# Kernel tuning notes

Measured on AMD Instinct MI355X. Metric: run time of the kernel, lower is better.

## Reference

```python
import jax, jax.numpy as jnp
import numpy as np

T = 2048          # num tokens (prefill)
H = 4096          # hidden_size
NH = 32           # num query heads
NKV = 8           # num kv heads (GQA)
HD = H // NH      # head_dim = 128
BASE = 1000000.0  # rope_theta
NEG = -1e30


def _rope(x, positions):
    # NeoX-style rotary embedding (vLLM default). x: [T, nh, HD]
    half = HD // 2
    inv_freq = 1.0 / (BASE ** (jnp.arange(half, dtype=jnp.float32) / half))
    freqs = positions.astype(jnp.float32)[:, None] * inv_freq  # [T, half]
    cos = jnp.concatenate([jnp.cos(freqs), jnp.cos(freqs)], -1)[:, None, :]
    sin = jnp.concatenate([jnp.sin(freqs), jnp.sin(freqs)], -1)[:, None, :]
    rot = jnp.concatenate([-x[..., half:], x[..., :half]], -1)
    return x * cos + rot * sin


def setup_inputs() -> dict:
    key = jax.random.key(0)
    k1, k2, k3 = jax.random.split(key, 3)
    hidden_states = jax.random.normal(k1, (T, H), jnp.float32)
    wqkv = jax.random.normal(k2, (H, (NH + 2 * NKV) * HD), jnp.float32) * 0.02
    wo = jax.random.normal(k3, (NH * HD, H), jnp.float32) * 0.02
    positions = jnp.arange(T, dtype=jnp.int32)
    return {"positions": positions, "hidden_states": hidden_states,
            "wqkv": wqkv, "wo": wo}


def reference(positions, hidden_states, wqkv, wo):
    # fused QKV projection
    qkv = hidden_states @ wqkv                      # [T, (NH+2*NKV)*HD]
    q, k, v = jnp.split(qkv, [NH * HD, NH * HD + NKV * HD], axis=-1)
    q = q.reshape(T, NH, HD)
    k = k.reshape(T, NKV, HD)
    v = v.reshape(T, NKV, HD)
    # inline RoPE on q, k
    q = _rope(q, positions)
    k = _rope(k, positions)
    # GQA: expand kv heads to query heads
    rep = NH // NKV
    k = jnp.repeat(k, rep, axis=1)                  # [T, NH, HD]
    v = jnp.repeat(v, rep, axis=1)
    # causal scaled dot-product attention (prefill path of PagedAttention)
    scores = jnp.einsum('qhd,khd->hqk', q, k) * (HD ** -0.5)  # [NH, T, T]
    causal = positions[:, None] >= positions[None, :]          # [T, T]
    scores = jnp.where(causal[None, :, :], scores, NEG)
    probs = jax.nn.softmax(scores, axis=-1)
    attn = jnp.einsum('hqk,khd->qhd', probs, v).reshape(T, NH * HD)
    return attn @ wo
```

## Files before the change

### kernel.cpp

```cpp
#include <hip/hip_runtime.h>
#include <hip/hip_bf16.h>

typedef __attribute__((ext_vector_type(8))) short bf16x8;
typedef __attribute__((ext_vector_type(4))) float f32x4;
typedef unsigned short u16;

#define T_TOK 2048
#define HID 4096
#define NH 32
#define NKV 8
#define HD 128
#define QKVN 6144
#define KOFF 4096
#define VOFF 5120
#define ATTN_SCALE 0.08838834764831845f

static __device__ __forceinline__ float bf2f(u16 x) {
    union { float f; unsigned u; } v; v.u = ((unsigned)x) << 16; return v.f;
}
static __device__ __forceinline__ u16 f2bf(float f) {
    union { float f; unsigned u; } v; v.f = f;
    unsigned u = v.u;
    unsigned r = (u + 0x7fff + ((u >> 16) & 1)) >> 16;
    return (u16)r;
}

static __device__ __forceinline__ void gload16(const u16* g, u16* l) {
    __builtin_amdgcn_global_load_lds((const __attribute__((address_space(1))) void*)g,
                                     (__attribute__((address_space(3))) void*)l, 16, 0, 0);
}

#define VMC(n) asm volatile("s_waitcnt vmcnt(%0)" :: "i"(n) : "memory")

__global__ __launch_bounds__(256) void convk(const float* __restrict__ in, u16* __restrict__ out) {
    int i = blockIdx.x * 256 + threadIdx.x;
    float4 v = ((const float4*)in)[i];
    ushort4 o;
    o.x = f2bf(v.x); o.y = f2bf(v.y); o.z = f2bf(v.z); o.w = f2bf(v.w);
    ((ushort4*)out)[i] = o;
}

__global__ __launch_bounds__(256) void transpk(const float* __restrict__ in, u16* __restrict__ out,
                                               int R, int C) {
    __shared__ float tile[64][65];
    int c0 = blockIdx.x * 64, r0 = blockIdx.y * 64;
    int tid = threadIdx.x;
#pragma unroll
    for (int it = 0; it < 4; ++it) {
        int ci = it * 256 + tid;
        int r = ci >> 4, c4 = (ci & 15) * 4;
        float4 v = *(const float4*)&in[(size_t)(r0 + r) * C + c0 + c4];
        tile[r][c4 + 0] = v.x; tile[r][c4 + 1] = v.y; tile[r][c4 + 2] = v.z; tile[r][c4 + 3] = v.w;
    }
    __syncthreads();
#pragma unroll
    for (int it = 0; it < 4; ++it) {
        int ci = it * 256 + tid;
        int c = ci >> 4, rq = (ci & 15) * 4;
        ushort4 o;
        o.x = f2bf(tile[rq + 0][c]); o.y = f2bf(tile[rq + 1][c]);
        o.z = f2bf(tile[rq + 2][c]); o.w = f2bf(tile[rq + 3][c]);
        *(ushort4*)&out[(size_t)(c0 + c) * R + r0 + rq] = o;
    }
}

template <int BN, int OUTF32>
__global__ __launch_bounds__(512) void gemm8p(const u16* __restrict__ A, const u16* __restrict__ Bt,
                                              void* __restrict__ Cout, int M, int N, int K) {
    constexpr int BM = 256, BK = 32;
    constexpr int WN = BN / 4;
    constexpr int NF = WN / 16;
    constexpr int BCH = BN / 16;
    constexpr int CA = 2 + (BCH + 7) / 8;
    constexpr int CB = 2 + BCH / 8;
    constexpr int ABUF = BM * BK;
    constexpr int BBUF = BN * BK;
    constexpr int BUFSZ = ABUF + BBUF;

    __shared__ __attribute__((aligned(16))) u16 lds[4 * BUFSZ];

    int bid = blockIdx.x;
    int m0 = (bid & 7) * BM, n0 = (bid >> 3) * BN;
    int tid = threadIdx.x, lane = tid & 63, wid = tid >> 6;
    int wm = wid >> 2, wn = wid & 3;
    int l15 = lane & 15, g4 = lane >> 4;
    int srow = lane >> 2;
    int sslot = (lane & 3) ^ ((lane >> 3) & 3);
    int swz = (g4 ^ ((l15 >> 1) & 3)) * 8;
    int NK = K / BK;
    bool shortw = (CA != CB) && (wid >= 4);

    auto STAGE = [&](int kt, int c) {
        u16* base = &lds[(kt & 3) * BUFSZ];
        size_t kcol = (size_t)kt * BK + sslot * 8;
        if (c < 2) {
            int ch = wid * 2 + c;
            gload16(&A[(size_t)(m0 + ch * 16 + srow) * K + kcol], base + ch * 512);
        } else {
            int ch = (c - 2) * 8 + wid;
            if (ch < BCH)
                gload16(&Bt[(size_t)(n0 + ch * 16 + srow) * K + kcol], base + ABUF + ch * 512);
        }
    };

    f32x4 acc[8][NF];
#pragma unroll
    for (int i = 0; i < 8; ++i)
#pragma unroll
        for (int j = 0; j < NF; ++j) acc[i][j] = (f32x4){0.f, 0.f, 0.f, 0.f};

    for (int t = 0; t < 3; ++t)
        for (int c = 0; c < CA; ++c) STAGE(t, c);
    if (shortw) VMC(2 * CB); else VMC(2 * CA);
    __builtin_amdgcn_s_barrier();
    __builtin_amdgcn_sched_barrier(0);

    for (int g = 0; g < NK; ++g) {
        const u16* ab = &lds[(g & 3) * BUFSZ];
        const u16* bb = ab + ABUF;

        bf16x8 bfr[NF], af[4];
#pragma unroll
        for (int j = 0; j < NF; ++j)
            bfr[j] = *(const bf16x8*)&bb[(wn * WN + j * 16 + l15) * BK + swz];
#pragma unroll
        for (int i = 0; i < 4; ++i)
            af[i] = *(const bf16x8*)&ab[(wm * 128 + i * 16 + l15) * BK + swz];
        if (g + 3 < NK) {
            STAGE(g + 3, 0); STAGE(g + 3, 1);
        }
        __builtin_amdgcn_s_setprio(1);
#pragma unroll
        for (int i = 0; i < 4; ++i)
#pragma unroll
            for (int j = 0; j < NF; ++j)
                acc[i][j] = __builtin_amdgcn_mfma_f32_16x16x32_bf16(af[i], bfr[j], acc[i][j], 0, 0, 0);
        __builtin_amdgcn_s_setprio(0);

        bf16x8 af2[4];
#pragma unroll
        for (int i = 0; i < 4; ++i)
            af2[i] = *(const bf16x8*)&ab[(wm * 128 + (4 + i) * 16 + l15) * BK + swz];
        if (g + 3 < NK) {
#pragma unroll
            for (int c = 2; c < CA; ++c) STAGE(g + 3, c);
        }
        __builtin_amdgcn_s_setprio(1);
#pragma unroll
        for (int i = 0; i < 4; ++i)
#pragma unroll
            for (int j = 0; j < NF; ++j)
                acc[4 + i][j] = __builtin_amdgcn_mfma_f32_16x16x32_bf16(af2[i], bfr[j], acc[4 + i][j], 0, 0, 0);
        __builtin_amdgcn_s_setprio(0);

        if (g < NK - 3)       { if (shortw) VMC(2 * CB); else VMC(2 * CA); }
        else if (g == NK - 3) { if (shortw) VMC(CB);     else VMC(CA); }
        else if (g == NK - 2) VMC(0);
        __builtin_amdgcn_s_barrier();
        __builtin_amdgcn_sched_barrier(0);
    }

#pragma unroll
    for (int mi = 0; mi < 8; ++mi)
#pragma unroll
        for (int j = 0; j < NF; ++j)
#pragma unroll
            for (int i = 0; i < 4; ++i) {
                int row = m0 + wm * 128 + mi * 16 + g4 * 4 + i;
                int col = n0 + wn * WN + j * 16 + l15;
                float v = acc[mi][j][i];
                if (OUTF32) ((float*)Cout)[(size_t)row * N + col] = v;
                else        ((u16*)Cout)[(size_t)row * N + col] = f2bf(v);
            }
}

__global__ __launch_bounds__(256) void ropek(u16* __restrict__ qkvb, const int* __restrict__ positions) {
    __shared__ float cs_[64], sn_[64];
    int t = blockIdx.x;
    float pos = (float)positions[t];
    if (threadIdx.x < 64) {
        int d = threadIdx.x;
        float inv = exp2f(-(float)d * (19.931568569324174f / 64.0f));
        float fr = pos * inv;
        cs_[d] = cosf(fr);
        sn_[d] = sinf(fr);
    }
    __syncthreads();
#pragma unroll
    for (int it = 0; it < 10; ++it) {
        int ci = it * 256 + threadIdx.x;
        int hh = ci >> 6, d = ci & 63;
        int base = (hh < NH) ? hh * HD : KOFF + (hh - NH) * HD;
        size_t off = (size_t)t * QKVN + base + d;
        float x1 = bf2f(qkvb[off]);
        float x2 = bf2f(qkvb[off + 64]);
        float s = sn_[d], c = cs_[d];
        float y1 = x1 * c - x2 * s;
        float y2 = x2 * c + x1 * s;
        if (hh < NH) { y1 *= ATTN_SCALE; y2 *= ATTN_SCALE; }
        qkvb[off]      = f2bf(y1);
        qkvb[off + 64] = f2bf(y2);
    }
}

__global__ __launch_bounds__(256) void vtranspk(const u16* __restrict__ qkvb, u16* __restrict__ vT) {
    __shared__ __attribute__((aligned(16))) u16 tile[64][136];
    int kvh = blockIdx.x, t0 = blockIdx.y * 64;
    int tid = threadIdx.x;
#pragma unroll
    for (int it = 0; it < 4; ++it) {
        int ci = it * 256 + tid;
        int r = ci >> 4, c8 = (ci & 15) * 8;
        *(bf16x8*)&tile[r][c8] = *(const bf16x8*)&qkvb[(size_t)(t0 + r) * QKVN + VOFF + kvh * HD + c8];
    }
    __syncthreads();
#pragma unroll
    for (int it = 0; it < 4; ++it) {
        int ci = it * 256 + tid;
        int d = ci >> 3, tc = (ci & 7) * 8;
        union { bf16x8 v; u16 u[8]; } o;
#pragma unroll
        for (int e = 0; e < 8; ++e) o.u[e] = tile[tc + e][d];
        *(bf16x8*)&vT[((size_t)kvh * HD + d) * T_TOK + t0 + tc] = o.v;
    }
}

__global__ __launch_bounds__(256) void attnk(const u16* __restrict__ qkvb, const u16* __restrict__ vT,
                                             u16* __restrict__ attnb) {
    __shared__ __attribute__((aligned(16))) u16 kt_[64 * 136];
    __shared__ __attribute__((aligned(16))) u16 vt_[128 * 72];
    __shared__ __attribute__((aligned(16))) u16 pl_[4 * 16 * 72];
    int h = blockIdx.x, qt = 31 - blockIdx.y;
    int kvh = h >> 2;
    int q0 = qt * 64;
    int tid = threadIdx.x, lane = tid & 63, wid = tid >> 6;
    int l15 = lane & 15, g = lane >> 4;

    int kr = tid >> 4, kc = (tid & 15) * 8;
    int vd = tid >> 3, vc = (tid & 7) * 8;
    const u16* kbase = qkvb + KOFF + (size_t)kvh * HD + kc;
    const u16* vbase = vT + ((size_t)kvh * HD) * T_TOK + vc;

    bf16x8 qf[4];
    int qrow = q0 + wid * 16 + l15;
#pragma unroll
    for (int ks = 0; ks < 4; ++ks)
        qf[ks] = *(const bf16x8*)&qkvb[(size_t)qrow * QKVN + h * HD + ks * 32 + g * 8];

    f32x4 o[8];
#pragma unroll
    for (int df = 0; df < 8; ++df) o[df] = (f32x4){0.f, 0.f, 0.f, 0.f};
    float m_run[4], l_run[4];
#pragma unroll
    for (int i = 0; i < 4; ++i) { m_run[i] = -3.0e38f; l_run[i] = 0.f; }

    bf16x8 kreg[4], vreg[4];
#pragma unroll
    for (int it = 0; it < 4; ++it)
        kreg[it] = *(const bf16x8*)&kbase[(size_t)(it * 16 + kr) * QKVN];
#pragma unroll
    for (int it = 0; it < 4; ++it)
        vreg[it] = *(const bf16x8*)&vbase[(size_t)(it * 32 + vd) * T_TOK];
#pragma unroll
    for (int it = 0; it < 4; ++it) *(bf16x8*)&kt_[(it * 16 + kr) * 136 + kc] = kreg[it];
#pragma unroll
    for (int it = 0; it < 4; ++it) *(bf16x8*)&vt_[(it * 32 + vd) * 72 + vc] = vreg[it];
    {
        int ktl = (1 <= qt) ? 1 : qt;
#pragma unroll
        for (int it = 0; it < 4; ++it)
            kreg[it] = *(const bf16x8*)&kbase[(size_t)(ktl * 64 + it * 16 + kr) * QKVN];
#pragma unroll
        for (int it = 0; it < 4; ++it)
            vreg[it] = *(const bf16x8*)&vbase[(size_t)(it * 32 + vd) * T_TOK + ktl * 64];
    }
    __syncthreads();

    for (int kt2 = 0; kt2 <= qt; ++kt2) {
        int kvb = kt2 * 64;
        bool diag = (kt2 == qt);

        f32x4 s[4];
#pragma unroll
        for (int nf = 0; nf < 4; ++nf) s[nf] = (f32x4){0.f, 0.f, 0.f, 0.f};
        __builtin_amdgcn_s_setprio(1);
#pragma unroll
        for (int ks = 0; ks < 4; ++ks) {
#pragma unroll
            for (int nf = 0; nf < 4; ++nf) {
                bf16x8 bfr = *(const bf16x8*)&kt_[(nf * 16 + l15) * 136 + ks * 32 + g * 8];
                s[nf] = __builtin_amdgcn_mfma_f32_16x16x32_bf16(qf[ks], bfr, s[nf], 0, 0, 0);
            }
        }
        __builtin_amdgcn_s_setprio(0);

        float mrow[4];
#pragma unroll
        for (int i = 0; i < 4; ++i) {
            int qr = q0 + wid * 16 + g * 4 + i;
            float mx = -3.0e38f;
#pragma unroll
            for (int nf = 0; nf < 4; ++nf) {
                float v = s[nf][i];
                if (diag) {
                    int kvc = kvb + nf * 16 + l15;
                    v = (kvc <= qr) ? v : -1.0e30f;
                    s[nf][i] = v;
                }
                mx = fmaxf(mx, v);
            }
            mrow[i] = mx;
        }
#pragma unroll
        for (int dd = 1; dd < 16; dd <<= 1)
#pragma unroll
            for (int i = 0; i < 4; ++i) mrow[i] = fmaxf(mrow[i], __shfl_xor(mrow[i], dd));

        int ok = 1;
#pragma unroll
        for (int i = 0; i < 4; ++i) ok &= (mrow[i] <= m_run[i] + 8.0f) ? 1 : 0;
        if (!__all(ok)) {
            float alpha[4];
#pragma unroll
            for (int i = 0; i < 4; ++i) {
                float mnew = fmaxf(m_run[i], mrow[i]);
                alpha[i] = __expf(m_run[i] - mnew);
                m_run[i] = mnew;
                l_run[i] *= alpha[i];
            }
#pragma unroll
            for (int df = 0; df < 8; ++df)
#pragma unroll
                for (int i = 0; i < 4; ++i) o[df][i] *= alpha[i];
        }

        float rsum[4] = {0.f, 0.f, 0.f, 0.f};
#pragma unroll
        for (int nf = 0; nf < 4; ++nf)
#pragma unroll
            for (int i = 0; i < 4; ++i) {
                float p = __expf(s[nf][i] - m_run[i]);
                rsum[i] += p;
                pl_[wid * 1152 + (g * 4 + i) * 72 + nf * 16 + l15] = f2bf(p);
            }
#pragma unroll
        for (int dd = 1; dd < 16; dd <<= 1)
#pragma unroll
            for (int i = 0; i < 4; ++i) rsum[i] += __shfl_xor(rsum[i], dd);
#pragma unroll
        for (int i = 0; i < 4; ++i) l_run[i] += rsum[i];

        __builtin_amdgcn_s_setprio(1);
#pragma unroll
        for (int ks2 = 0; ks2 < 2; ++ks2) {
            bf16x8 af = *(const bf16x8*)&pl_[wid * 1152 + l15 * 72 + ks2 * 32 + g * 8];
#pragma unroll
            for (int df = 0; df < 8; ++df) {
                bf16x8 bfr = *(const bf16x8*)&vt_[(df * 16 + l15) * 72 + ks2 * 32 + g * 8];
                o[df] = __builtin_amdgcn_mfma_f32_16x16x32_bf16(af, bfr, o[df], 0, 0, 0);
            }
        }
        __builtin_amdgcn_s_setprio(0);

        if (kt2 < qt) {
            __syncthreads();
#pragma unroll
            for (int it = 0; it < 4; ++it) *(bf16x8*)&kt_[(it * 16 + kr) * 136 + kc] = kreg[it];
#pragma unroll
            for (int it = 0; it < 4; ++it) *(bf16x8*)&vt_[(it * 32 + vd) * 72 + vc] = vreg[it];
            int ktl = (kt2 + 2 <= qt) ? kt2 + 2 : qt;
#pragma unroll
            for (int it = 0; it < 4; ++it)
                kreg[it] = *(const bf16x8*)&kbase[(size_t)(ktl * 64 + it * 16 + kr) * QKVN];
#pragma unroll
            for (int it = 0; it < 4; ++it)
                vreg[it] = *(const bf16x8*)&vbase[(size_t)(it * 32 + vd) * T_TOK + ktl * 64];
            __syncthreads();
        }
    }

#pragma unroll
    for (int df = 0; df < 8; ++df)
#pragma unroll
        for (int i = 0; i < 4; ++i) {
            int qr = q0 + wid * 16 + g * 4 + i;
            int col = h * HD + df * 16 + l15;
            attnb[(size_t)qr * (NH * HD) + col] = f2bf(o[df][i] / l_run[i]);
        }
}

extern "C" void kernel_launch(void* const* d_in, const int* in_sizes, int n_in,
                              void* d_out, int out_size, void* d_ws, size_t ws_size,
                              hipStream_t stream) {
    const int*   positions = (const int*)d_in[0];
    const float* hs        = (const float*)d_in[1];
    const float* wqkv      = (const float*)d_in[2];
    const float* wo        = (const float*)d_in[3];
    float* out = (float*)d_out;

    char* ws = (char*)d_ws;
    u16* hsb   = (u16*)(ws);
    u16* wqkvT = (u16*)(ws + 16777216);
    u16* woT   = (u16*)(ws + 16777216 + 50331648);
    u16* qkvb  = (u16*)(ws + 16777216 + 50331648 + 33554432);
    u16* vT    = (u16*)(ws + 16777216 + 50331648 + 33554432 + 25165824);
    u16* attnb = hsb;

    convk<<<8192, 256, 0, stream>>>(hs, hsb);
    transpk<<<dim3(96, 64), 256, 0, stream>>>(wqkv, wqkvT, HID, QKVN);
    transpk<<<dim3(64, 64), 256, 0, stream>>>(wo, woT, HID, HID);

    gemm8p<192, 0><<<dim3(256), 512, 0, stream>>>(hsb, wqkvT, qkvb, T_TOK, QKVN, HID);

    ropek<<<T_TOK, 256, 0, stream>>>(qkvb, positions);

    vtranspk<<<dim3(NKV, 32), 256, 0, stream>>>(qkvb, vT);

    attnk<<<dim3(NH, 32), 256, 0, stream>>>(qkvb, vT, attnb);

    gemm8p<128, 1><<<dim3(256), 512, 0, stream>>>(attnb, woT, out, T_TOK, HID, HID);
}
```

Measured before the change: 339.6 us.

## Enlarge attention query tile to 128 rows with 8 waves sharing K/V tiles

The attention kernel now runs 512 threads (8 waves) per block covering 128 query rows instead of 64, so each K/V tile loaded into shared memory is reused by twice as many waves. Waves whose rows lie entirely above a KV tile skip compute through a per-wave active flag, and the diagonal mask applies per wave. This halves global K/V traffic per query and the block count, in exchange for idle waves near the diagonal, more barrier participants, and fewer blocks for load balancing on the causal triangle.

```diff
diff --git a/kernel.cpp b/kernel.cpp
--- a/kernel.cpp
+++ b/kernel.cpp
@@ -225,21 +225,19 @@
     }
 }
 
-__global__ __launch_bounds__(256) void attnk(const u16* __restrict__ qkvb, const u16* __restrict__ vT,
+__global__ __launch_bounds__(512) void attnk(const u16* __restrict__ qkvb, const u16* __restrict__ vT,
                                              u16* __restrict__ attnb) {
     __shared__ __attribute__((aligned(16))) u16 kt_[64 * 136];
     __shared__ __attribute__((aligned(16))) u16 vt_[128 * 72];
-    __shared__ __attribute__((aligned(16))) u16 pl_[4 * 16 * 72];
-    int h = blockIdx.x, qt = 31 - blockIdx.y;
+    __shared__ __attribute__((aligned(16))) u16 pl_[8 * 16 * 72];
+    int h = blockIdx.x, qt = 15 - blockIdx.y;
     int kvh = h >> 2;
-    int q0 = qt * 64;
+    int q0 = qt * 128;
     int tid = threadIdx.x, lane = tid & 63, wid = tid >> 6;
     int l15 = lane & 15, g = lane >> 4;
 
-    int kr = tid >> 4, kc = (tid & 15) * 8;
-    int vd = tid >> 3, vc = (tid & 7) * 8;
-    const u16* kbase = qkvb + KOFF + (size_t)kvh * HD + kc;
-    const u16* vbase = vT + ((size_t)kvh * HD) * T_TOK + vc;
+    const u16* kbase = qkvb + KOFF + (size_t)kvh * HD;
+    const u16* vbase = vT + (size_t)kvh * HD * T_TOK;
 
     bf16x8 qf[4];
     int qrow = q0 + wid * 16 + l15;
@@ -254,127 +252,133 @@
 #pragma unroll
     for (int i = 0; i < 4; ++i) { m_run[i] = -3.0e38f; l_run[i] = 0.f; }
 
-    bf16x8 kreg[4], vreg[4];
-#pragma unroll
-    for (int it = 0; it < 4; ++it)
-        kreg[it] = *(const bf16x8*)&kbase[(size_t)(it * 16 + kr) * QKVN];
-#pragma unroll
-    for (int it = 0; it < 4; ++it)
-        vreg[it] = *(const bf16x8*)&vbase[(size_t)(it * 32 + vd) * T_TOK];
-#pragma unroll
-    for (int it = 0; it < 4; ++it) *(bf16x8*)&kt_[(it * 16 + kr) * 136 + kc] = kreg[it];
-#pragma unroll
-    for (int it = 0; it < 4; ++it) *(bf16x8*)&vt_[(it * 32 + vd) * 72 + vc] = vreg[it];
-    {
-        int ktl = (1 <= qt) ? 1 : qt;
-#pragma unroll
-        for (int it = 0; it < 4; ++it)
-            kreg[it] = *(const bf16x8*)&kbase[(size_t)(ktl * 64 + it * 16 + kr) * QKVN];
-#pragma unroll
-        for (int it = 0; it < 4; ++it)
-            vreg[it] = *(const bf16x8*)&vbase[(size_t)(it * 32 + vd) * T_TOK + ktl * 64];
+    int NT = 2 * qt + 2;
+
+    bf16x8 kreg[2], vreg[2];
+#pragma unroll
+    for (int it = 0; it < 2; ++it) {
+        int gi = it * 512 + tid;
+        kreg[it] = *(const bf16x8*)&kbase[(size_t)(gi >> 4) * QKVN + (gi & 15) * 8];
+        vreg[it] = *(const bf16x8*)&vbase[(size_t)(gi >> 3) * T_TOK + (gi & 7) * 8];
+    }
+#pragma unroll
+    for (int it = 0; it < 2; ++it) {
+        int gi = it * 512 + tid;
+        *(bf16x8*)&kt_[(gi >> 4) * 136 + (gi & 15) * 8] = kreg[it];
+        *(bf16x8*)&vt_[(gi >> 3) * 72 + (gi & 7) * 8] = vreg[it];
+    }
+#pragma unroll
+    for (int it = 0; it < 2; ++it) {
+        int gi = it * 512 + tid;
+        kreg[it] = *(const bf16x8*)&kbase[(size_t)(64 + (gi >> 4)) * QKVN + (gi & 15) * 8];
+        vreg[it] = *(const bf16x8*)&vbase[(size_t)(gi >> 3) * T_TOK + 64 + (gi & 7) * 8];
     }
     __syncthreads();
 
-    for (int kt2 = 0; kt2 <= qt; ++kt2) {
+    for (int kt2 = 0; kt2 < NT; ++kt2) {
         int kvb = kt2 * 64;
-        bool diag = (kt2 == qt);
-
-        f32x4 s[4];
-#pragma unroll
-        for (int nf = 0; nf < 4; ++nf) s[nf] = (f32x4){0.f, 0.f, 0.f, 0.f};
-        __builtin_amdgcn_s_setprio(1);
-#pragma unroll
-        for (int ks = 0; ks < 4; ++ks) {
-#pragma unroll
-            for (int nf = 0; nf < 4; ++nf) {
-                bf16x8 bfr = *(const bf16x8*)&kt_[(nf * 16 + l15) * 136 + ks * 32 + g * 8];
-                s[nf] = __builtin_amdgcn_mfma_f32_16x16x32_bf16(qf[ks], bfr, s[nf], 0, 0, 0);
-            }
-        }
-        __builtin_amdgcn_s_setprio(0);
-
-        float mrow[4];
-#pragma unroll
-        for (int i = 0; i < 4; ++i) {
-            int qr = q0 + wid * 16 + g * 4 + i;
-            float mx = -3.0e38f;
-#pragma unroll
-            for (int nf = 0; nf < 4; ++nf) {
-                float v = s[nf][i];
-                if (diag) {
-                    int kvc = kvb + nf * 16 + l15;
-                    v = (kvc <= qr) ? v : -1.0e30f;
-                    s[nf][i] = v;
+        bool active = (kvb <= q0 + wid * 16 + 15);
+        bool diag   = (kvb + 63 > q0 + wid * 16);
+
+        if (active) {
+            f32x4 s[4];
+#pragma unroll
+            for (int nf = 0; nf < 4; ++nf) s[nf] = (f32x4){0.f, 0.f, 0.f, 0.f};
+            __builtin_amdgcn_s_setprio(1);
+#pragma unroll
+            for (int ks = 0; ks < 4; ++ks) {
+#pragma unroll
+                for (int nf = 0; nf < 4; ++nf) {
+                    bf16x8 bfr = *(const bf16x8*)&kt_[(nf * 16 + l15) * 136 + ks * 32 + g * 8];
+                    s[nf] = __builtin_amdgcn_mfma_f32_16x16x32_bf16(qf[ks], bfr, s[nf], 0, 0, 0);
                 }
-                mx = fmaxf(mx, v);
-            }
-            mrow[i] = mx;
-        }
-#pragma unroll
-        for (int dd = 1; dd < 16; dd <<= 1)
-#pragma unroll
-            for (int i = 0; i < 4; ++i) mrow[i] = fmaxf(mrow[i], __shfl_xor(mrow[i], dd));
-
-        int ok = 1;
-#pragma unroll
-        for (int i = 0; i < 4; ++i) ok &= (mrow[i] <= m_run[i] + 8.0f) ? 1 : 0;
-        if (!__all(ok)) {
-            float alpha[4];
+            }
+            __builtin_amdgcn_s_setprio(0);
+
+            float mrow[4];
 #pragma unroll
             for (int i = 0; i < 4; ++i) {
-                float mnew = fmaxf(m_run[i], mrow[i]);
-                alpha[i] = __expf(m_run[i] - mnew);
-                m_run[i] = mnew;
-                l_run[i] *= alpha[i];
-            }
-#pragma unroll
-            for (int df = 0; df < 8; ++df)
-#pragma unroll
-                for (int i = 0; i < 4; ++i) o[df][i] *= alpha[i];
-        }
-
-        float rsum[4] = {0.f, 0.f, 0.f, 0.f};
-#pragma unroll
-        for (int nf = 0; nf < 4; ++nf)
-#pragma unroll
-            for (int i = 0; i < 4; ++i) {
-                float p = __expf(s[nf][i] - m_run[i]);
-                rsum[i] += p;
-                pl_[wid * 1152 + (g * 4 + i) * 72 + nf * 16 + l15] = f2bf(p);
-            }
-#pragma unroll
-        for (int dd = 1; dd < 16; dd <<= 1)
-#pragma unroll
-            for (int i = 0; i < 4; ++i) rsum[i] += __shfl_xor(rsum[i], dd);
-#pragma unroll
-        for (int i = 0; i < 4; ++i) l_run[i] += rsum[i];
-
-        __builtin_amdgcn_s_setprio(1);
-#pragma unroll
-        for (int ks2 = 0; ks2 < 2; ++ks2) {
-            bf16x8 af = *(const bf16x8*)&pl_[wid * 1152 + l15 * 72 + ks2 * 32 + g * 8];
-#pragma unroll
-            for (int df = 0; df < 8; ++df) {
-                bf16x8 bfr = *(const bf16x8*)&vt_[(df * 16 + l15) * 72 + ks2 * 32 + g * 8];
-                o[df] = __builtin_amdgcn_mfma_f32_16x16x32_bf16(af, bfr, o[df], 0, 0, 0);
-            }
-        }
-        __builtin_amdgcn_s_setprio(0);
-
-        if (kt2 < qt) {
+                int qr = q0 + wid * 16 + g * 4 + i;
+                float mx = -3.0e38f;
+#pragma unroll
+                for (int nf = 0; nf < 4; ++nf) {
+                    float v = s[nf][i];
+                    if (diag) {
+                        int kvc = kvb + nf * 16 + l15;
+                        v = (kvc <= qr) ? v : -1.0e30f;
+                        s[nf][i] = v;
+                    }
+                    mx = fmaxf(mx, v);
+                }
+                mrow[i] = mx;
+            }
+#pragma unroll
+            for (int dd = 1; dd < 16; dd <<= 1)
+#pragma unroll
+                for (int i = 0; i < 4; ++i) mrow[i] = fmaxf(mrow[i], __shfl_xor(mrow[i], dd));
+
+            int ok = 1;
+#pragma unroll
+            for (int i = 0; i < 4; ++i) ok &= (mrow[i] <= m_run[i] + 8.0f) ? 1 : 0;
+            if (!__all(ok)) {
+                float alpha[4];
+#pragma unroll
+                for (int i = 0; i < 4; ++i) {
+                    float mnew = fmaxf(m_run[i], mrow[i]);
+                    alpha[i] = __expf(m_run[i] - mnew);
+                    m_run[i] = mnew;
+                    l_run[i] *= alpha[i];
+                }
+#pragma unroll
+                for (int df = 0; df < 8; ++df)
+#pragma unroll
+                    for (int i = 0; i < 4; ++i) o[df][i] *= alpha[i];
+            }
+
+            float rsum[4] = {0.f, 0.f, 0.f, 0.f};
+#pragma unroll
+            for (int nf = 0; nf < 4; ++nf)
+#pragma unroll
+                for (int i = 0; i < 4; ++i) {
+                    float p = __expf(s[nf][i] - m_run[i]);
+                    rsum[i] += p;
+                    pl_[wid * 1152 + (g * 4 + i) * 72 + nf * 16 + l15] = f2bf(p);
+                }
+#pragma unroll
+            for (int dd = 1; dd < 16; dd <<= 1)
+#pragma unroll
+                for (int i = 0; i < 4; ++i) rsum[i] += __shfl_xor(rsum[i], dd);
+#pragma unroll
+            for (int i = 0; i < 4; ++i) l_run[i] += rsum[i];
+
+            __builtin_amdgcn_s_setprio(1);
+#pragma unroll
+            for (int ks2 = 0; ks2 < 2; ++ks2) {
+                bf16x8 af = *(const bf16x8*)&pl_[wid * 1152 + l15 * 72 + ks2 * 32 + g * 8];
+#pragma unroll
+                for (int df = 0; df < 8; ++df) {
+                    bf16x8 bfr = *(const bf16x8*)&vt_[(df * 16 + l15) * 72 + ks2 * 32 + g * 8];
+                    o[df] = __builtin_amdgcn_mfma_f32_16x16x32_bf16(af, bfr, o[df], 0, 0, 0);
+                }
+            }
+            __builtin_amdgcn_s_setprio(0);
+        }
+
+        if (kt2 < NT - 1) {
             __syncthreads();
 #pragma unroll
-            for (int it = 0; it < 4; ++it) *(bf16x8*)&kt_[(it * 16 + kr) * 136 + kc] = kreg[it];
-#pragma unroll
-            for (int it = 0; it < 4; ++it) *(bf16x8*)&vt_[(it * 32 + vd) * 72 + vc] = vreg[it];
-            int ktl = (kt2 + 2 <= qt) ? kt2 + 2 : qt;
-#pragma unroll
-            for (int it = 0; it < 4; ++it)
-                kreg[it] = *(const bf16x8*)&kbase[(size_t)(ktl * 64 + it * 16 + kr) * QKVN];
-#pragma unroll
-            for (int it = 0; it < 4; ++it)
-                vreg[it] = *(const bf16x8*)&vbase[(size_t)(it * 32 + vd) * T_TOK + ktl * 64];
+            for (int it = 0; it < 2; ++it) {
+                int gi = it * 512 + tid;
+                *(bf16x8*)&kt_[(gi >> 4) * 136 + (gi & 15) * 8] = kreg[it];
+                *(bf16x8*)&vt_[(gi >> 3) * 72 + (gi & 7) * 8] = vreg[it];
+            }
+            int ktl = (kt2 + 2 < NT) ? kt2 + 2 : NT - 1;
+#pragma unroll
+            for (int it = 0; it < 2; ++it) {
+                int gi = it * 512 + tid;
+                kreg[it] = *(const bf16x8*)&kbase[(size_t)(ktl * 64 + (gi >> 4)) * QKVN + (gi & 15) * 8];
+                vreg[it] = *(const bf16x8*)&vbase[(size_t)(gi >> 3) * T_TOK + ktl * 64 + (gi & 7) * 8];
+            }
             __syncthreads();
         }
     }
@@ -416,7 +420,7 @@
 
     vtranspk<<<dim3(NKV, 32), 256, 0, stream>>>(qkvb, vT);
 
-    attnk<<<dim3(NH, 32), 256, 0, stream>>>(qkvb, vT, attnb);
+    attnk<<<dim3(NH, 16), 512, 0, stream>>>(qkvb, vT, attnb);
 
     gemm8p<128, 1><<<dim3(256), 512, 0, stream>>>(attnb, woT, out, T_TOK, HID, HID);
 }
```

Measured after the change: 335.6 us. About the same (-1.2%).
